# Kernel optimization log

Hardware: AMD Instinct MI355X
Metric: run time of the kernel (lower is better)

The kernel has to match this reference:

```python
import math
import jax, jax.numpy as jnp
import numpy as np

B, S, D, H, HD = 32, 512, 768, 12, 64
K, ST = 2, 2  # pooling kernel / stride
NEG = jnp.float32(-10000.0)


def _alibi_slopes(n):
    def p2(m):
        start = 2 ** (-(2 ** (-(math.log2(m) - 3))))
        return [start * start ** i for i in range(m)]
    if math.log2(n).is_integer():
        return p2(n)
    c = 2 ** math.floor(math.log2(n))
    return p2(c) + _alibi_slopes(2 * c)[0::2][: n - c]


def _sum_pool(x, k, s, out_len):
    # x: [B, L, C]; ceil_mode sum-pool over axis 1 (zero padded on the right)
    pad = (out_len - 1) * s + k - x.shape[1]
    if pad > 0:
        x = jnp.pad(x, ((0, 0), (0, pad), (0, 0)))
    win = x[:, jnp.arange(out_len)[:, None] * s + jnp.arange(k)]  # [B, out, k, C]
    return win.sum(axis=2)


def setup_inputs() -> dict:
    key = jax.random.key(0)
    k1, k2, k3 = jax.random.split(key, 3)
    hidden_states = jax.random.normal(k1, (B, S, D), dtype=jnp.float32)
    lengths = jax.random.randint(k2, (B,), 128, S + 1)
    attention_mask = jnp.arange(S)[None, :] < lengths[:, None]  # bool [B,S]
    Wqkv_w = jax.random.normal(k3, (3 * D, D), dtype=jnp.float32) * 0.02
    Wqkv_b = jnp.zeros((3 * D,), dtype=jnp.float32)
    return {"hidden_states": hidden_states, "attention_mask": attention_mask,
            "Wqkv_w": Wqkv_w, "Wqkv_b": Wqkv_b}


def reference(hidden_states, attention_mask, Wqkv_w, Wqkv_b):
    b, s = attention_mask.shape
    qkv = hidden_states @ Wqkv_w.T + Wqkv_b  # [B,S,3D]
    qkv = qkv.reshape(b, s, 3, H, HD)        # '(t h d)' split order
    q = qkv[:, :, 0]                          # [B,S,H,HD]
    k = qkv[:, :, 1].transpose(0, 2, 1, 3)    # [B,H,S,HD]
    v = qkv[:, :, 2].transpose(0, 2, 1, 3)

    # MaskedAvgPool1d on queries (flattened heads), ceil_mode sum-pool / count
    kk = min(K, s)
    out_len = -(-(max(0, s - kk)) // ST) + 1
    q_flat = q.reshape(b, s, H * HD)
    q_flat = jnp.where(attention_mask[:, :, None], q_flat, 0.0)
    norm = _sum_pool(attention_mask.astype(jnp.float32)[:, :, None], kk, ST, out_len)  # [B,out,1]
    new_mask = norm[..., 0] != 0
    norm = jnp.where(norm == 0, 1.0, norm)
    q_pool = _sum_pool(q_flat, kk, ST, out_len) / norm  # [B,out,D]
    q = q_pool.reshape(b, out_len, H, HD).transpose(0, 2, 1, 3)  # [B,H,out,HD]

    # bias: 0 where (new_mask_q & mask_k), else -10000; plus ALiBi
    pair = new_mask[:, :, None] & attention_mask[:, None, :]  # [B,out,S]
    bias = jnp.where(pair, 0.0, NEG)[:, None, :, :]           # [B,1,out,S]
    rel = jnp.abs(jnp.arange(s)[None, :] - jnp.arange(out_len)[:, None])  # [out,S]
    slopes = jnp.asarray(_alibi_slopes(H), dtype=jnp.float32)
    alibi = slopes[:, None, None] * (-rel.astype(jnp.float32))  # [H,out,S]
    scores = jnp.einsum('bhqd,bhkd->bhqk', q, k) / math.sqrt(HD) + bias + alibi[None]
    attn = jax.nn.softmax(scores, axis=-1)
    out = jnp.einsum('bhqk,bhkd->bhqd', attn, v)  # [B,H,out,HD]
    out = out.transpose(0, 2, 1, 3).reshape(b, out_len, H * HD)
    return out, new_mask
```

## Files before the change

kernel.cpp:

```cpp
#include <hip/hip_runtime.h>

#define BB 32
#define SS 512
#define DD 768
#define HH 12
#define HDIM 64
#define OL 256
#define NQKV 2304
#define GM (BB*SS)

#define NEG2 (-14426.9504089f)

typedef __bf16 bf16_t;
typedef bf16_t bf16x8 __attribute__((ext_vector_type(8)));
typedef float f32x4 __attribute__((ext_vector_type(4)));
typedef unsigned short u16x8 __attribute__((ext_vector_type(8)));

__device__ __forceinline__ unsigned short f2bf(float f) {
  unsigned u = __float_as_uint(f);
  u = u + 0x7FFFu + ((u >> 16) & 1u);
  return (unsigned short)(u >> 16);
}
__device__ __forceinline__ float b2f(unsigned short s) {
  return __uint_as_float(((unsigned)s) << 16);
}

__global__ __launch_bounds__(256) void prep_all(
    const float* __restrict__ hidden,
    const void* __restrict__ mraw,
    const float* __restrict__ W,
    unsigned short* __restrict__ Btb,
    unsigned short* __restrict__ Abf,
    unsigned short* __restrict__ Apool,
    float* __restrict__ kbias,
    float* __restrict__ invn,
    unsigned char* __restrict__ nmask,
    float* __restrict__ out_nm) {
  const int blk = blockIdx.x;
  const int t = threadIdx.x;
  const unsigned char* mb = (const unsigned char*)mraw;

  if (blk < 1728) {
    const int i = blk * 256 + t;
    float4 v = ((const float4*)W)[i];
    ushort4 o;
    o.x = f2bf(v.x); o.y = f2bf(v.y); o.z = f2bf(v.z); o.w = f2bf(v.w);
    ((ushort4*)Btb)[i] = o;
  } else if (blk < 1792) {
    const int idx = (blk - 1728) * 256 + t;
    const int b = idx >> 9, s = idx & 511;
    const bool isbyte = (mb[1] != 0);
    const int mv = isbyte ? (int)(mb[idx] != 0) : (int)(((const int*)mraw)[idx] != 0);
    kbias[idx] = mv ? 0.f : NEG2;
    if (s < OL) {
      const int i0 = b * SS + 2 * s, i1 = i0 + 1;
      const int m0 = isbyte ? (int)(mb[i0] != 0) : (int)(((const int*)mraw)[i0] != 0);
      const int m1 = isbyte ? (int)(mb[i1] != 0) : (int)(((const int*)mraw)[i1] != 0);
      const int n = m0 + m1;
      invn[b * OL + s] = (n > 0) ? 1.f / (float)n : 1.f;
      nmask[b * OL + s] = (n > 0) ? 1 : 0;
      out_nm[b * OL + s] = (n > 0) ? 1.f : 0.f;
    }
  } else {
    const int i = (blk - 1792) * 256 + t;
    const int c = (i % 192) * 4;
    const int ol = i / 192;
    const int b = ol >> 8, o = ol & 255;
    const int s0 = b * SS + 2 * o;
    const bool isbyte = (mb[1] != 0);
    const int m0 = isbyte ? (int)(mb[s0] != 0) : (int)(((const int*)mraw)[s0] != 0);
    const int m1 = isbyte ? (int)(mb[s0 + 1] != 0) : (int)(((const int*)mraw)[s0 + 1] != 0);
    const int n = m0 + m1;
    const float inv = (n > 0) ? 1.f / (float)n : 1.f;
    const float m0v = (float)m0, m1v = (float)m1;
    const float4 h0 = *(const float4*)(hidden + (size_t)s0 * DD + c);
    const float4 h1 = *(const float4*)(hidden + (size_t)(s0 + 1) * DD + c);
    ushort4 a0, a1, ap;
    a0.x = f2bf(h0.x); a0.y = f2bf(h0.y); a0.z = f2bf(h0.z); a0.w = f2bf(h0.w);
    a1.x = f2bf(h1.x); a1.y = f2bf(h1.y); a1.z = f2bf(h1.z); a1.w = f2bf(h1.w);
    ap.x = f2bf((h0.x * m0v + h1.x * m1v) * inv);
    ap.y = f2bf((h0.y * m0v + h1.y * m1v) * inv);
    ap.z = f2bf((h0.z * m0v + h1.z * m1v) * inv);
    ap.w = f2bf((h0.w * m0v + h1.w * m1v) * inv);
    *(ushort4*)(Abf + (size_t)s0 * DD + c) = a0;
    *(ushort4*)(Abf + (size_t)(s0 + 1) * DD + c) = a1;
    *(ushort4*)(Apool + (size_t)ol * DD + c) = ap;
  }
}

#define NT 12
__global__ __launch_bounds__(256, 2) void gemm_qkv(
    const unsigned short* __restrict__ A,
    const unsigned short* __restrict__ Apool,
    const unsigned short* __restrict__ Bt,
    const float* __restrict__ bias,
    unsigned short* __restrict__ Kbuf,
    unsigned short* __restrict__ qp,
    unsigned short* __restrict__ vT,
    const unsigned char* __restrict__ nmask) {
  __shared__ __align__(16) char smem[65536];

  const int t = threadIdx.x;
  const int lane = t & 63;
  const int w = t >> 6;
  const int wm = w >> 1, wn = w & 1;
  const int fr = lane & 15, hi = lane >> 4;

  const int p = blockIdx.x;
  const int l = (p & 7) * 240 + (p >> 3);
  const bool isQ = l >= 1536;
  int m0, n0;
  if (!isQ) { m0 = (l / 12) * 128; n0 = 768 + (l % 12) * 128; }
  else      { const int l2 = l - 1536; m0 = (l2 / 6) * 128; n0 = (l2 % 6) * 128; }
  const unsigned short* Asel = isQ ? Apool : A;

  f32x4 acc[4][4] = {};

  const int sr8 = lane >> 3;
  const int sx8 = ((lane & 7) ^ sr8) * 8;
  const int wq = __builtin_amdgcn_readfirstlane(w);
  const unsigned short* aSrc = Asel + (size_t)(m0 + wq * 32 + sr8) * DD + sx8;
  const unsigned short* bSrc = Bt + (size_t)(n0 + wq * 32 + sr8) * DD + sx8;

#define GLOAD(SRC, DST)                                                        \
  __builtin_amdgcn_global_load_lds(                                           \
      (const __attribute__((address_space(1))) unsigned int*)(SRC),           \
      (__attribute__((address_space(3))) unsigned int*)(DST), 16, 0, 0)

#define STAGE(T) do {                                                          \
    char* da_ = smem + ((T) & 1) * 32768;                                      \
    char* db_ = da_ + 16384;                                                   \
    const unsigned short* as_ = aSrc + (T) * 64;                               \
    const unsigned short* bs_ = bSrc + (T) * 64;                               \
    _Pragma("unroll")                                                          \
    for (int i_ = 0; i_ < 4; ++i_) {                                           \
      GLOAD(as_ + (size_t)i_ * 8 * DD, da_ + (wq * 32 + i_ * 8) * 128);        \
      GLOAD(bs_ + (size_t)i_ * 8 * DD, db_ + (wq * 32 + i_ * 8) * 128);        \
    }                                                                          \
  } while (0)

  STAGE(0);
  STAGE(1);

  const int cb0 = (hi * 16) ^ ((fr & 7) << 4);
  const int cb1 = (64 + hi * 16) ^ ((fr & 7) << 4);

  for (int kt = 0; kt < NT; ++kt) {
    if (kt < NT - 1) {
      asm volatile("s_waitcnt vmcnt(8)" ::: "memory");
    } else {
      asm volatile("s_waitcnt vmcnt(0)" ::: "memory");
    }
    __builtin_amdgcn_sched_barrier(0);
    __builtin_amdgcn_s_barrier();
    __builtin_amdgcn_sched_barrier(0);

    const char* bA = smem + (kt & 1) * 32768;
    const char* bB = bA + 16384;

    bf16x8 a0[4], b0[4], a1[4], b1[4];
#pragma unroll
    for (int f = 0; f < 4; ++f) {
      a0[f] = *(const bf16x8*)(bA + (wm * 64 + f * 16 + fr) * 128 + cb0);
      b0[f] = *(const bf16x8*)(bB + (wn * 64 + f * 16 + fr) * 128 + cb0);
    }
    __builtin_amdgcn_sched_barrier(0);
#pragma unroll
    for (int f = 0; f < 4; ++f) {
      a1[f] = *(const bf16x8*)(bA + (wm * 64 + f * 16 + fr) * 128 + cb1);
      b1[f] = *(const bf16x8*)(bB + (wn * 64 + f * 16 + fr) * 128 + cb1);
    }
    asm volatile("s_waitcnt lgkmcnt(8)" ::: "memory");
    __builtin_amdgcn_sched_barrier(0);
    __builtin_amdgcn_s_setprio(1);
#pragma unroll
    for (int mf = 0; mf < 4; ++mf)
#pragma unroll
      for (int nf = 0; nf < 4; ++nf)
        acc[mf][nf] = __builtin_amdgcn_mfma_f32_16x16x32_bf16(
            a0[mf], b0[nf], acc[mf][nf], 0, 0, 0);
    __builtin_amdgcn_s_setprio(0);
    asm volatile("s_waitcnt lgkmcnt(0)" ::: "memory");
    __builtin_amdgcn_sched_barrier(0);
    __builtin_amdgcn_s_barrier();
    __builtin_amdgcn_sched_barrier(0);
    if (kt + 2 < NT) STAGE(kt + 2);
    __builtin_amdgcn_sched_barrier(0);
    __builtin_amdgcn_s_setprio(1);
#pragma unroll
    for (int mf = 0; mf < 4; ++mf)
#pragma unroll
      for (int nf = 0; nf < 4; ++nf)
        acc[mf][nf] = __builtin_amdgcn_mfma_f32_16x16x32_bf16(
            a1[mf], b1[nf], acc[mf][nf], 0, 0, 0);
    __builtin_amdgcn_s_setprio(0);
  }
#undef STAGE
#undef GLOAD

  if (isQ) {
#pragma unroll
    for (int mf = 0; mf < 4; ++mf) {
      const int r0 = m0 + wm * 64 + mf * 16 + hi * 4;
      const uchar4 nm = *(const uchar4*)&nmask[r0];
      const float g0 = nm.x ? 1.f : 0.f;
      const float g1 = nm.y ? 1.f : 0.f;
      const float g2 = nm.z ? 1.f : 0.f;
      const float g3 = nm.w ? 1.f : 0.f;
#pragma unroll
      for (int nf = 0; nf < 4; ++nf) {
        const int gnc = n0 + wn * 64 + nf * 16 + fr;
        const float bvs = bias[gnc];
        const f32x4 a = acc[mf][nf];
        qp[(size_t)(r0 + 0) * 768 + gnc] = f2bf((a[0] + bvs) * g0);
        qp[(size_t)(r0 + 1) * 768 + gnc] = f2bf((a[1] + bvs) * g1);
        qp[(size_t)(r0 + 2) * 768 + gnc] = f2bf((a[2] + bvs) * g2);
        qp[(size_t)(r0 + 3) * 768 + gnc] = f2bf((a[3] + bvs) * g3);
      }
    }
  } else if (n0 < 1536) {
#pragma unroll
    for (int nf = 0; nf < 4; ++nf) {
      const int nc = wn * 64 + nf * 16 + fr;
      const float bvs = bias[n0 + nc];
      const int gnc = n0 - 768 + nc;
#pragma unroll
      for (int mf = 0; mf < 4; ++mf) {
        const int gmr = m0 + wm * 64 + mf * 16 + hi * 4;
#pragma unroll
        for (int j = 0; j < 4; ++j)
          Kbuf[(size_t)(gmr + j) * 768 + gnc] = f2bf(acc[mf][nf][j] + bvs);
      }
    }
  } else {
    const int b = m0 >> 9;
    const int s0 = m0 & 511;
    unsigned short* lt = (unsigned short*)smem;
#pragma unroll
    for (int nf = 0; nf < 4; ++nf) {
      const int nl = wn * 64 + nf * 16 + fr;
      const float bvs = bias[n0 + nl];
#pragma unroll
      for (int mf = 0; mf < 4; ++mf) {
        const int mb = wm * 64 + mf * 16 + hi * 4;
        ushort4 pk;
        pk.x = f2bf(acc[mf][nf][0] + bvs);
        pk.y = f2bf(acc[mf][nf][1] + bvs);
        pk.z = f2bf(acc[mf][nf][2] + bvs);
        pk.w = f2bf(acc[mf][nf][3] + bvs);
        *(ushort4*)&lt[nl * 136 + mb] = pk;
      }
    }
    __syncthreads();
#pragma unroll
    for (int i = 0; i < 8; ++i) {
      const int row = i * 16 + (t >> 4);
      const int ch = t & 15;
      const u16x8 v = *(const u16x8*)&lt[row * 136 + ch * 8];
      const int n = n0 - 1536 + row;
      const int h2 = n >> 6, d2 = n & 63;
      *(u16x8*)(vT + ((size_t)((b * HH + h2) * HDIM + d2)) * 512 + s0 + ch * 8) = v;
    }
  }
}

__constant__ float c_slopes2[12] = {
    0.72134752f, 0.36067376f, 0.18033688f, 0.09016844f,
    0.04508422f, 0.02254211f, 0.011271055f, 0.0056355275f,
    1.02013945f, 0.51006972f, 0.25503486f, 0.12751743f};

__global__ __launch_bounds__(512, 4) void attn_mfma(
    const unsigned short* __restrict__ qp,
    const unsigned short* __restrict__ Kb,
    const unsigned short* __restrict__ vT,
    const float* __restrict__ kbias,
    const unsigned char* __restrict__ nmask,
    float* __restrict__ out) {
  __shared__ __align__(16) char smem[51200];
  const int t = threadIdx.x;
  const int lane = t & 63;
  const int w = t >> 6;
  const int wq = __builtin_amdgcn_readfirstlane(w);
  const int fr = lane & 15, hi = lane >> 4;

  const int p = blockIdx.x;
  const int l = (p & 7) * 96 + (p >> 3);
  const int qb = l & 1;
  const int bh = l >> 1;
  const int h = bh % HH, b = bh / HH;
  const int q0 = qb * 128 + wq * 16;

  char* ptb = smem + 32768 + wq * 2048;
  float* kbl = (float*)(smem + 49152);

  const int srow = lane >> 3;
  const int scol = ((lane & 7) ^ srow) * 8;

#define GLOAD(SRC, DST)                                                        \
  __builtin_amdgcn_global_load_lds(                                           \
      (const __attribute__((address_space(1))) unsigned int*)(SRC),           \
      (__attribute__((address_space(3))) unsigned int*)(DST), 16, 0, 0)

  if (wq == 0) {
    GLOAD(kbias + b * SS + lane * 4, smem + 49152);
    GLOAD(kbias + b * SS + 256 + lane * 4, smem + 50176);
  }

  bf16x8 qf[2];
#pragma unroll
  for (int ks = 0; ks < 2; ++ks)
    qf[ks] = *(const bf16x8*)(qp + (size_t)(b * OL + q0 + fr) * DD +
                              h * HDIM + ks * 32 + hi * 8);

  int nmv = (int)nmask[b * OL + q0 + (lane & 15)];
  int qmbits = 0;
#pragma unroll
  for (int j = 0; j < 4; ++j)
    if (__shfl(nmv, hi * 4 + j, 64)) qmbits |= 1 << j;

  const float slope2 = c_slopes2[h];
  f32x4 oacc[4] = {};
  float lpart[4] = {};

#define STAGE(TILE, BUF) do {                                                  \
    char* kd_ = smem + (BUF) * 8192 + wq * 1024;                               \
    char* vd_ = smem + 16384 + (BUF) * 8192 + wq * 1024;                       \
    const unsigned short* ks_ =                                                \
        Kb + (size_t)(b * SS + (TILE) * 64 + wq * 8 + srow) * 768 + h * HDIM + scol; \
    const unsigned short* vs_ =                                                \
        vT + (size_t)((b * HH + h) * HDIM + wq * 8 + srow) * SS + (TILE) * 64 + scol; \
    GLOAD(ks_, kd_);                                                           \
    GLOAD(vs_, vd_);                                                           \
  } while (0)

  __builtin_amdgcn_sched_barrier(0);
  STAGE(0, 0);
  STAGE(1, 1);
  __builtin_amdgcn_sched_barrier(0);

  for (int tile = 0; tile < 8; ++tile) {
    const int cur = tile & 1;
    const int key0 = tile * 64;
    if (tile < 7) {
      asm volatile("s_waitcnt vmcnt(2)" ::: "memory");
    } else {
      asm volatile("s_waitcnt vmcnt(0)" ::: "memory");
    }
    __builtin_amdgcn_sched_barrier(0);
    __builtin_amdgcn_s_barrier();
    __builtin_amdgcn_sched_barrier(0);

    char* ktb = smem + cur * 8192;
    char* vtb = smem + 16384 + cur * 8192;

    f32x4 sacc[4] = {};
#pragma unroll
    for (int ks = 0; ks < 2; ++ks) {
      bf16x8 kf[4];
#pragma unroll
      for (int n = 0; n < 4; ++n) {
        const int by = ((n * 16 + fr) * 128 + (ks * 64 + hi * 16)) ^ ((fr & 7) << 4);
        kf[n] = *(const bf16x8*)(ktb + by);
      }
#pragma unroll
      for (int n = 0; n < 4; ++n)
        sacc[n] = __builtin_amdgcn_mfma_f32_16x16x32_bf16(qf[ks], kf[n], sacc[n], 0, 0, 0);
    }

    float kbv[4], keyfv[4];
#pragma unroll
    for (int n = 0; n < 4; ++n) {
      kbv[n] = kbl[key0 + n * 16 + fr];
      keyfv[n] = (float)(key0 + n * 16 + fr);
    }
#pragma unroll
    for (int j = 0; j < 4; ++j) {
      const bool qm = (qmbits >> j) & 1;
      const float qvf = (float)(q0 + hi * 4 + j);
      float lp = lpart[j];
#pragma unroll
      for (int n = 0; n < 4; ++n) {
        const float biasv = qm ? kbv[n] : 0.f;
        const float rel = fabsf(keyfv[n] - qvf);
        float tv = fmaf(sacc[n][j], 0.18033688011f, biasv);
        tv = fmaf(rel, -slope2, tv);
        float pe;
        asm("v_exp_f32 %0, %1" : "=v"(pe) : "v"(tv));
        lp += pe;
        const int by = ((hi * 4 + j) * 128 + (n * 16 + fr) * 2) ^
                       (((hi * 4 + j) & 7) << 4);
        *(unsigned short*)(ptb + by) = f2bf(pe);
      }
      lpart[j] = lp;
    }
    asm volatile("s_waitcnt lgkmcnt(0)" ::: "memory");
    __builtin_amdgcn_sched_barrier(0);

#pragma unroll
    for (int ks = 0; ks < 2; ++ks) {
      bf16x8 pf, vf[4];
      {
        const int by = (fr * 128 + (ks * 64 + hi * 16)) ^ ((fr & 7) << 4);
        pf = *(const bf16x8*)(ptb + by);
      }
#pragma unroll
      for (int nd = 0; nd < 4; ++nd) {
        const int by = ((nd * 16 + fr) * 128 + (ks * 64 + hi * 16)) ^ ((fr & 7) << 4);
        vf[nd] = *(const bf16x8*)(vtb + by);
      }
#pragma unroll
      for (int nd = 0; nd < 4; ++nd)
        oacc[nd] = __builtin_amdgcn_mfma_f32_16x16x32_bf16(pf, vf[nd], oacc[nd], 0, 0, 0);
    }

    __builtin_amdgcn_sched_barrier(0);
    __builtin_amdgcn_s_barrier();
    __builtin_amdgcn_sched_barrier(0);
    if (tile + 2 < 8) STAGE(tile + 2, cur);
  }
#undef STAGE
#undef GLOAD

  float* ot = (float*)(smem + wq * 4352);
#pragma unroll
  for (int j = 0; j < 4; ++j) {
    float lv = lpart[j];
    lv += __shfl_xor(lv, 1, 64);
    lv += __shfl_xor(lv, 2, 64);
    lv += __shfl_xor(lv, 4, 64);
    lv += __shfl_xor(lv, 8, 64);
    const float rl = 1.f / lv;
    const int row = hi * 4 + j;
#pragma unroll
    for (int nd = 0; nd < 4; ++nd)
      ot[row * 68 + nd * 16 + fr] = oacc[nd][j] * rl;
  }
  asm volatile("s_waitcnt lgkmcnt(0)" ::: "memory");
  __builtin_amdgcn_sched_barrier(0);
#pragma unroll
  for (int i = 0; i < 4; ++i) {
    const int idx = i * 64 + lane;
    const int row = idx >> 4, c4 = idx & 15;
    const float4 v = *(const float4*)&ot[row * 68 + c4 * 4];
    *(float4*)(out + (size_t)(b * OL + q0 + row) * DD + h * HDIM + c4 * 4) = v;
  }
}

extern "C" void kernel_launch(void* const* d_in, const int* in_sizes, int n_in,
                              void* d_out, int out_size, void* d_ws, size_t ws_size,
                              hipStream_t stream) {
  const float* hidden = (const float*)d_in[0];
  const void* maskraw = d_in[1];
  const float* W = (const float*)d_in[2];
  const float* bias = (const float*)d_in[3];
  float* out = (float*)d_out;

  char* ws = (char*)d_ws;
  unsigned short* Abf   = (unsigned short*)(ws);
  unsigned short* Btb   = (unsigned short*)(ws + 25165824);
  unsigned short* Kbuf  = (unsigned short*)(ws + 28704768);
  unsigned short* vT    = (unsigned short*)(ws + 53870592);
  unsigned short* qp    = (unsigned short*)(ws + 79036416);
  float* kbias          = (float*)(ws + 91619328);
  float* invn           = (float*)(ws + 91684864);
  unsigned char* nmask  = (unsigned char*)(ws + 91717632);
  unsigned short* Apool = (unsigned short*)(ws + 91725824);

  float* out_nm = out + (size_t)BB * OL * DD;

  prep_all<<<7936, 256, 0, stream>>>(hidden, maskraw, W, Btb, Abf, Apool,
                                     kbias, invn, nmask, out_nm);
  gemm_qkv<<<1920, 256, 0, stream>>>(Abf, Apool, Btb, bias, Kbuf, qp, vT, nmask);
  attn_mfma<<<768, 512, 0, stream>>>(qp, Kbuf, vT, kbias, nmask, out);
}
```

Baseline: 96.62 us.

## Enlarge QKV GEMM tiles to 256x256 with 8 waves per block

Result: slower. 103.7 us (+7.3%).

```diff
diff --git a/kernel.cpp b/kernel.cpp
--- a/kernel.cpp
+++ b/kernel.cpp
@@ -88,8 +88,7 @@
   }
 }
 
-#define NT 12
-__global__ __launch_bounds__(256, 2) void gemm_qkv(
+__global__ __launch_bounds__(512, 2) void gemm_qkv(
     const unsigned short* __restrict__ A,
     const unsigned short* __restrict__ Apool,
     const unsigned short* __restrict__ Bt,
@@ -98,110 +97,139 @@
     unsigned short* __restrict__ qp,
     unsigned short* __restrict__ vT,
     const unsigned char* __restrict__ nmask) {
-  __shared__ __align__(16) char smem[65536];
+  __shared__ __align__(16) char smem[131072];
 
   const int t = threadIdx.x;
   const int lane = t & 63;
   const int w = t >> 6;
-  const int wm = w >> 1, wn = w & 1;
+  const int wm = w >> 2;
+  const int wn = w & 3;
   const int fr = lane & 15, hi = lane >> 4;
 
   const int p = blockIdx.x;
-  const int l = (p & 7) * 240 + (p >> 3);
-  const bool isQ = l >= 1536;
+  const int l = (p & 7) * 60 + (p >> 3);
+  const bool isQ = l >= 384;
   int m0, n0;
-  if (!isQ) { m0 = (l / 12) * 128; n0 = 768 + (l % 12) * 128; }
-  else      { const int l2 = l - 1536; m0 = (l2 / 6) * 128; n0 = (l2 % 6) * 128; }
+  if (!isQ) { m0 = (l / 6) * 256; n0 = 768 + (l % 6) * 256; }
+  else      { const int l2 = l - 384; m0 = (l2 / 3) * 256; n0 = (l2 % 3) * 256; }
   const unsigned short* Asel = isQ ? Apool : A;
 
-  f32x4 acc[4][4] = {};
+  f32x4 acc[8][4] = {};
 
   const int sr8 = lane >> 3;
   const int sx8 = ((lane & 7) ^ sr8) * 8;
   const int wq = __builtin_amdgcn_readfirstlane(w);
-  const unsigned short* aSrc = Asel + (size_t)(m0 + wq * 32 + sr8) * DD + sx8;
-  const unsigned short* bSrc = Bt + (size_t)(n0 + wq * 32 + sr8) * DD + sx8;
+  const unsigned short* aS = Asel + (size_t)(m0 + wq * 32 + sr8) * DD + sx8;
+  const unsigned short* bS = Bt + (size_t)(n0 + wq * 32 + sr8) * DD + sx8;
 
 #define GLOAD(SRC, DST)                                                        \
   __builtin_amdgcn_global_load_lds(                                           \
       (const __attribute__((address_space(1))) unsigned int*)(SRC),           \
       (__attribute__((address_space(3))) unsigned int*)(DST), 16, 0, 0)
 
-#define STAGE(T) do {                                                          \
-    char* da_ = smem + ((T) & 1) * 32768;                                      \
-    char* db_ = da_ + 16384;                                                   \
-    const unsigned short* as_ = aSrc + (T) * 64;                               \
-    const unsigned short* bs_ = bSrc + (T) * 64;                               \
+#define STAGE(KT) do {                                                         \
+    char* da_ = smem + ((KT) & 1) * 65536;                                     \
+    char* db_ = da_ + 32768;                                                   \
+    const unsigned short* as_ = aS + (KT) * 64;                                \
+    const unsigned short* bs_ = bS + (KT) * 64;                                \
     _Pragma("unroll")                                                          \
-    for (int i_ = 0; i_ < 4; ++i_) {                                           \
-      GLOAD(as_ + (size_t)i_ * 8 * DD, da_ + (wq * 32 + i_ * 8) * 128);        \
-      GLOAD(bs_ + (size_t)i_ * 8 * DD, db_ + (wq * 32 + i_ * 8) * 128);        \
+    for (int q_ = 0; q_ < 4; ++q_) {                                           \
+      GLOAD(as_ + (size_t)(8 * q_) * DD, da_ + (wq * 32 + 8 * q_) * 128);      \
+      GLOAD(bs_ + (size_t)(8 * q_) * DD, db_ + (wq * 32 + 8 * q_) * 128);      \
     }                                                                          \
   } while (0)
+
+#define SBAR()                                                                 \
+  do {                                                                         \
+    __builtin_amdgcn_sched_barrier(0);                                         \
+    __builtin_amdgcn_s_barrier();                                              \
+    __builtin_amdgcn_sched_barrier(0);                                         \
+  } while (0)
+
+#define LGKM0() do {                                                           \
+    asm volatile("s_waitcnt lgkmcnt(0)" ::: "memory");                          \
+    __builtin_amdgcn_sched_barrier(0);                                         \
+  } while (0)
+
+#define RDA(BA, MFH, CB)                                                       \
+  do {                                                                         \
+    _Pragma("unroll")                                                          \
+    for (int f_ = 0; f_ < 4; ++f_)                                             \
+      af[f_] = *(const bf16x8*)((BA) + (wm * 128 + (MFH) * 64 + f_ * 16 + fr) * 128 + (CB)); \
+  } while (0)
+
+#define RDB(BBF, CB)                                                           \
+  do {                                                                         \
+    _Pragma("unroll")                                                          \
+    for (int f_ = 0; f_ < 4; ++f_)                                             \
+      bf[f_] = *(const bf16x8*)((BBF) + (wn * 64 + f_ * 16 + fr) * 128 + (CB)); \
+  } while (0)
+
+#define MFMA16(MFH)                                                            \
+  do {                                                                         \
+    __builtin_amdgcn_s_setprio(1);                                             \
+    _Pragma("unroll")                                                          \
+    for (int mf_ = 0; mf_ < 4; ++mf_)                                          \
+      _Pragma("unroll")                                                        \
+      for (int nf_ = 0; nf_ < 4; ++nf_)                                        \
+        acc[(MFH) * 4 + mf_][nf_] = __builtin_amdgcn_mfma_f32_16x16x32_bf16(   \
+            af[mf_], bf[nf_], acc[(MFH) * 4 + mf_][nf_], 0, 0, 0);             \
+    __builtin_amdgcn_s_setprio(0);                                             \
+  } while (0)
+
+  const int cb0 = (hi * 16) ^ ((fr & 7) << 4);
+  const int cb1 = (64 + hi * 16) ^ ((fr & 7) << 4);
 
   STAGE(0);
   STAGE(1);
-
-  const int cb0 = (hi * 16) ^ ((fr & 7) << 4);
-  const int cb1 = (64 + hi * 16) ^ ((fr & 7) << 4);
-
-  for (int kt = 0; kt < NT; ++kt) {
-    if (kt < NT - 1) {
+  asm volatile("s_waitcnt vmcnt(8)" ::: "memory");
+  SBAR();
+
+  for (int kt = 0; kt < 12; ++kt) {
+    char* bA = smem + (kt & 1) * 65536;
+    char* bB = bA + 32768;
+    bf16x8 af[4], bf[4];
+
+    RDA(bA, 0, cb0); RDB(bB, cb0);
+    SBAR(); LGKM0();
+    MFMA16(0);
+    SBAR();
+
+    RDA(bA, 1, cb0);
+    SBAR(); LGKM0();
+    MFMA16(1);
+    SBAR();
+
+    RDA(bA, 0, cb1); RDB(bB, cb1);
+    SBAR(); LGKM0();
+    MFMA16(0);
+    SBAR();
+
+    RDA(bA, 1, cb1);
+    LGKM0();
+    SBAR();
+    if (kt < 10) STAGE(kt + 2);
+    __builtin_amdgcn_sched_barrier(0);
+    MFMA16(1);
+    if (kt < 10) {
       asm volatile("s_waitcnt vmcnt(8)" ::: "memory");
-    } else {
+    } else if (kt == 10) {
       asm volatile("s_waitcnt vmcnt(0)" ::: "memory");
     }
-    __builtin_amdgcn_sched_barrier(0);
-    __builtin_amdgcn_s_barrier();
-    __builtin_amdgcn_sched_barrier(0);
-
-    const char* bA = smem + (kt & 1) * 32768;
-    const char* bB = bA + 16384;
-
-    bf16x8 a0[4], b0[4], a1[4], b1[4];
-#pragma unroll
-    for (int f = 0; f < 4; ++f) {
-      a0[f] = *(const bf16x8*)(bA + (wm * 64 + f * 16 + fr) * 128 + cb0);
-      b0[f] = *(const bf16x8*)(bB + (wn * 64 + f * 16 + fr) * 128 + cb0);
-    }
-    __builtin_amdgcn_sched_barrier(0);
-#pragma unroll
-    for (int f = 0; f < 4; ++f) {
-      a1[f] = *(const bf16x8*)(bA + (wm * 64 + f * 16 + fr) * 128 + cb1);
-      b1[f] = *(const bf16x8*)(bB + (wn * 64 + f * 16 + fr) * 128 + cb1);
-    }
-    asm volatile("s_waitcnt lgkmcnt(8)" ::: "memory");
-    __builtin_amdgcn_sched_barrier(0);
-    __builtin_amdgcn_s_setprio(1);
-#pragma unroll
-    for (int mf = 0; mf < 4; ++mf)
-#pragma unroll
-      for (int nf = 0; nf < 4; ++nf)
-        acc[mf][nf] = __builtin_amdgcn_mfma_f32_16x16x32_bf16(
-            a0[mf], b0[nf], acc[mf][nf], 0, 0, 0);
-    __builtin_amdgcn_s_setprio(0);
-    asm volatile("s_waitcnt lgkmcnt(0)" ::: "memory");
-    __builtin_amdgcn_sched_barrier(0);
-    __builtin_amdgcn_s_barrier();
-    __builtin_amdgcn_sched_barrier(0);
-    if (kt + 2 < NT) STAGE(kt + 2);
-    __builtin_amdgcn_sched_barrier(0);
-    __builtin_amdgcn_s_setprio(1);
-#pragma unroll
-    for (int mf = 0; mf < 4; ++mf)
-#pragma unroll
-      for (int nf = 0; nf < 4; ++nf)
-        acc[mf][nf] = __builtin_amdgcn_mfma_f32_16x16x32_bf16(
-            a1[mf], b1[nf], acc[mf][nf], 0, 0, 0);
-    __builtin_amdgcn_s_setprio(0);
-  }
+    SBAR();
+  }
+#undef RDA
+#undef RDB
+#undef MFMA16
+#undef LGKM0
+#undef SBAR
 #undef STAGE
 #undef GLOAD
 
   if (isQ) {
 #pragma unroll
-    for (int mf = 0; mf < 4; ++mf) {
-      const int r0 = m0 + wm * 64 + mf * 16 + hi * 4;
+    for (int mf = 0; mf < 8; ++mf) {
+      const int r0 = m0 + wm * 128 + mf * 16 + hi * 4;
       const uchar4 nm = *(const uchar4*)&nmask[r0];
       const float g0 = nm.x ? 1.f : 0.f;
       const float g1 = nm.y ? 1.f : 0.f;
@@ -225,8 +253,8 @@
       const float bvs = bias[n0 + nc];
       const int gnc = n0 - 768 + nc;
 #pragma unroll
-      for (int mf = 0; mf < 4; ++mf) {
-        const int gmr = m0 + wm * 64 + mf * 16 + hi * 4;
+      for (int mf = 0; mf < 8; ++mf) {
+        const int gmr = m0 + wm * 128 + mf * 16 + hi * 4;
 #pragma unroll
         for (int j = 0; j < 4; ++j)
           Kbuf[(size_t)(gmr + j) * 768 + gnc] = f2bf(acc[mf][nf][j] + bvs);
@@ -235,31 +263,39 @@
   } else {
     const int b = m0 >> 9;
     const int s0 = m0 & 511;
-    unsigned short* lt = (unsigned short*)smem;
-#pragma unroll
-    for (int nf = 0; nf < 4; ++nf) {
-      const int nl = wn * 64 + nf * 16 + fr;
-      const float bvs = bias[n0 + nl];
-#pragma unroll
-      for (int mf = 0; mf < 4; ++mf) {
-        const int mb = wm * 64 + mf * 16 + hi * 4;
-        ushort4 pk;
-        pk.x = f2bf(acc[mf][nf][0] + bvs);
-        pk.y = f2bf(acc[mf][nf][1] + bvs);
-        pk.z = f2bf(acc[mf][nf][2] + bvs);
-        pk.w = f2bf(acc[mf][nf][3] + bvs);
-        *(ushort4*)&lt[nl * 136 + mb] = pk;
-      }
-    }
-    __syncthreads();
-#pragma unroll
-    for (int i = 0; i < 8; ++i) {
-      const int row = i * 16 + (t >> 4);
-      const int ch = t & 15;
-      const u16x8 v = *(const u16x8*)&lt[row * 136 + ch * 8];
-      const int n = n0 - 1536 + row;
-      const int h2 = n >> 6, d2 = n & 63;
-      *(u16x8*)(vT + ((size_t)((b * HH + h2) * HDIM + d2)) * 512 + s0 + ch * 8) = v;
+    const int h2 = ((n0 - 1536) >> 6) + wn;
+    unsigned short* tile = (unsigned short*)(smem + wq * 9216);
+    float bvs[4];
+#pragma unroll
+    for (int nf = 0; nf < 4; ++nf) bvs[nf] = bias[n0 + wn * 64 + nf * 16 + fr];
+#pragma unroll
+    for (int mh = 0; mh < 2; ++mh) {
+#pragma unroll
+      for (int nf = 0; nf < 4; ++nf) {
+        const int d = nf * 16 + fr;
+#pragma unroll
+        for (int mf2 = 0; mf2 < 4; ++mf2) {
+          const int mf = mh * 4 + mf2;
+          ushort4 pk;
+          pk.x = f2bf(acc[mf][nf][0] + bvs[nf]);
+          pk.y = f2bf(acc[mf][nf][1] + bvs[nf]);
+          pk.z = f2bf(acc[mf][nf][2] + bvs[nf]);
+          pk.w = f2bf(acc[mf][nf][3] + bvs[nf]);
+          *(ushort4*)&tile[d * 72 + mf2 * 16 + hi * 4] = pk;
+        }
+      }
+      asm volatile("s_waitcnt lgkmcnt(0)" ::: "memory");
+      __builtin_amdgcn_sched_barrier(0);
+      const int sb = s0 + wm * 128 + mh * 64;
+#pragma unroll
+      for (int i = 0; i < 8; ++i) {
+        const int task = i * 64 + lane;
+        const int d = task >> 3, ch = task & 7;
+        const u16x8 v = *(const u16x8*)&tile[d * 72 + ch * 8];
+        *(u16x8*)(vT + ((size_t)((b * HH + h2) * HDIM + d)) * 512 + sb + ch * 8) = v;
+      }
+      asm volatile("s_waitcnt lgkmcnt(0)" ::: "memory");
+      __builtin_amdgcn_sched_barrier(0);
     }
   }
 }
@@ -470,6 +506,6 @@
 
   prep_all<<<7936, 256, 0, stream>>>(hidden, maskraw, W, Btb, Abf, Apool,
                                      kbias, invn, nmask, out_nm);
-  gemm_qkv<<<1920, 256, 0, stream>>>(Abf, Apool, Btb, bias, Kbuf, qp, vT, nmask);
+  gemm_qkv<<<480, 512, 0, stream>>>(Abf, Apool, Btb, bias, Kbuf, qp, vT, nmask);
   attn_mfma<<<768, 512, 0, stream>>>(qp, Kbuf, vT, kbias, nmask, out);
 }
```

## Load GEMM B operand directly into registers, keep only A in LDS

Applied to the files above, without the earlier changes.

New measurement: 155.0 us. +60.4%, slower.

```diff
diff --git a/kernel.cpp b/kernel.cpp
--- a/kernel.cpp
+++ b/kernel.cpp
@@ -98,7 +98,7 @@
     unsigned short* __restrict__ qp,
     unsigned short* __restrict__ vT,
     const unsigned char* __restrict__ nmask) {
-  __shared__ __align__(16) char smem[65536];
+  __shared__ __align__(16) char smem[34816];
 
   const int t = threadIdx.x;
   const int lane = t & 63;
@@ -120,82 +120,96 @@
   const int sx8 = ((lane & 7) ^ sr8) * 8;
   const int wq = __builtin_amdgcn_readfirstlane(w);
   const unsigned short* aSrc = Asel + (size_t)(m0 + wq * 32 + sr8) * DD + sx8;
-  const unsigned short* bSrc = Bt + (size_t)(n0 + wq * 32 + sr8) * DD + sx8;
+  const unsigned short* bBase = Bt + (size_t)(n0 + wn * 64 + fr) * DD + hi * 8;
 
 #define GLOAD(SRC, DST)                                                        \
   __builtin_amdgcn_global_load_lds(                                           \
       (const __attribute__((address_space(1))) unsigned int*)(SRC),           \
       (__attribute__((address_space(3))) unsigned int*)(DST), 16, 0, 0)
 
-#define STAGE(T) do {                                                          \
-    char* da_ = smem + ((T) & 1) * 32768;                                      \
-    char* db_ = da_ + 16384;                                                   \
+#define STAGEA(T) do {                                                         \
+    char* da_ = smem + ((T) & 1) * 16384;                                      \
     const unsigned short* as_ = aSrc + (T) * 64;                               \
-    const unsigned short* bs_ = bSrc + (T) * 64;                               \
     _Pragma("unroll")                                                          \
-    for (int i_ = 0; i_ < 4; ++i_) {                                           \
+    for (int i_ = 0; i_ < 4; ++i_)                                             \
       GLOAD(as_ + (size_t)i_ * 8 * DD, da_ + (wq * 32 + i_ * 8) * 128);        \
-      GLOAD(bs_ + (size_t)i_ * 8 * DD, db_ + (wq * 32 + i_ * 8) * 128);        \
+  } while (0)
+
+#define LOADB(REG, T) do {                                                     \
+    _Pragma("unroll")                                                          \
+    for (int nf_ = 0; nf_ < 4; ++nf_) {                                        \
+      (REG)[nf_ * 2 + 0] = *(const bf16x8*)(bBase + (size_t)nf_ * 16 * DD + (T) * 64);      \
+      (REG)[nf_ * 2 + 1] = *(const bf16x8*)(bBase + (size_t)nf_ * 16 * DD + (T) * 64 + 32); \
     }                                                                          \
   } while (0)
 
-  STAGE(0);
-  STAGE(1);
+#define SBO() __builtin_amdgcn_sched_barrier(0)
+
+#define MFMAH(AF, BR, KS)                                                      \
+  do {                                                                         \
+    __builtin_amdgcn_s_setprio(1);                                             \
+    _Pragma("unroll")                                                          \
+    for (int mf_ = 0; mf_ < 4; ++mf_)                                          \
+      _Pragma("unroll")                                                        \
+      for (int nf_ = 0; nf_ < 4; ++nf_)                                        \
+        acc[mf_][nf_] = __builtin_amdgcn_mfma_f32_16x16x32_bf16(               \
+            (AF)[mf_], (BR)[nf_ * 2 + (KS)], acc[mf_][nf_], 0, 0, 0);          \
+    __builtin_amdgcn_s_setprio(0);                                             \
+  } while (0)
 
   const int cb0 = (hi * 16) ^ ((fr & 7) << 4);
   const int cb1 = (64 + hi * 16) ^ ((fr & 7) << 4);
-
+  const int ar = (wm * 64 + fr) * 128;
+
+  bf16x8 bRA[8], bRB[8];
+
+  LOADB(bRA, 0);
+  STAGEA(0);
+  STAGEA(1);
+  LOADB(bRB, 1);
+
+#define ITER_BODY(KT, BREG)                                                    \
+  do {                                                                         \
+    const char* pA_ = smem + ((KT) & 1) * 16384;                               \
+    bf16x8 a0[4], a1[4];                                                       \
+    _Pragma("unroll")                                                          \
+    for (int f_ = 0; f_ < 4; ++f_) a0[f_] = *(const bf16x8*)(pA_ + ar + f_ * 2048 + cb0); \
+    _Pragma("unroll")                                                          \
+    for (int f_ = 0; f_ < 4; ++f_) a1[f_] = *(const bf16x8*)(pA_ + ar + f_ * 2048 + cb1); \
+    asm volatile("s_waitcnt lgkmcnt(4)" ::: "memory");                          \
+    SBO();                                                                     \
+    MFMAH(a0, BREG, 0);                                                        \
+    asm volatile("s_waitcnt lgkmcnt(0)" ::: "memory");                          \
+    SBO();                                                                     \
+    __builtin_amdgcn_s_barrier();         \
+    SBO();                                                                     \
+    if ((KT) < 10) STAGEA((KT) + 2);                                           \
+    SBO();                                                                     \
+    MFMAH(a1, BREG, 1);                                                        \
+    if ((KT) < 10) LOADB(BREG, (KT) + 2);          \
+  } while (0)
+
+#pragma unroll
   for (int kt = 0; kt < NT; ++kt) {
     if (kt < NT - 1) {
-      asm volatile("s_waitcnt vmcnt(8)" ::: "memory");
+      asm volatile("s_waitcnt vmcnt(12)" ::: "memory");
     } else {
       asm volatile("s_waitcnt vmcnt(0)" ::: "memory");
     }
-    __builtin_amdgcn_sched_barrier(0);
+    SBO();
     __builtin_amdgcn_s_barrier();
-    __builtin_amdgcn_sched_barrier(0);
-
-    const char* bA = smem + (kt & 1) * 32768;
-    const char* bB = bA + 16384;
-
-    bf16x8 a0[4], b0[4], a1[4], b1[4];
-#pragma unroll
-    for (int f = 0; f < 4; ++f) {
-      a0[f] = *(const bf16x8*)(bA + (wm * 64 + f * 16 + fr) * 128 + cb0);
-      b0[f] = *(const bf16x8*)(bB + (wn * 64 + f * 16 + fr) * 128 + cb0);
-    }
-    __builtin_amdgcn_sched_barrier(0);
-#pragma unroll
-    for (int f = 0; f < 4; ++f) {
-      a1[f] = *(const bf16x8*)(bA + (wm * 64 + f * 16 + fr) * 128 + cb1);
-      b1[f] = *(const bf16x8*)(bB + (wn * 64 + f * 16 + fr) * 128 + cb1);
-    }
-    asm volatile("s_waitcnt lgkmcnt(8)" ::: "memory");
-    __builtin_amdgcn_sched_barrier(0);
-    __builtin_amdgcn_s_setprio(1);
-#pragma unroll
-    for (int mf = 0; mf < 4; ++mf)
-#pragma unroll
-      for (int nf = 0; nf < 4; ++nf)
-        acc[mf][nf] = __builtin_amdgcn_mfma_f32_16x16x32_bf16(
-            a0[mf], b0[nf], acc[mf][nf], 0, 0, 0);
-    __builtin_amdgcn_s_setprio(0);
-    asm volatile("s_waitcnt lgkmcnt(0)" ::: "memory");
-    __builtin_amdgcn_sched_barrier(0);
-    __builtin_amdgcn_s_barrier();
-    __builtin_amdgcn_sched_barrier(0);
-    if (kt + 2 < NT) STAGE(kt + 2);
-    __builtin_amdgcn_sched_barrier(0);
-    __builtin_amdgcn_s_setprio(1);
-#pragma unroll
-    for (int mf = 0; mf < 4; ++mf)
-#pragma unroll
-      for (int nf = 0; nf < 4; ++nf)
-        acc[mf][nf] = __builtin_amdgcn_mfma_f32_16x16x32_bf16(
-            a1[mf], b1[nf], acc[mf][nf], 0, 0, 0);
-    __builtin_amdgcn_s_setprio(0);
-  }
-#undef STAGE
+    SBO();
+    if ((kt & 1) == 0) {
+      ITER_BODY(kt, bRA);
+    } else {
+      ITER_BODY(kt, bRB);
+    }
+  }
+#undef ITER_BODY
+#undef MFMAH
+#undef SBO
+#undef LOADB
+#undef STAGEA
 #undef GLOAD
 
   if (isQ) {
```
